# Kernel optimization log

Hardware: AMD Instinct MI355X
Metric: run time of the kernel (lower is better)

## Reference

```python
import jax, jax.numpy as jnp
import numpy as np

B, T, E, A = 16, 512, 256, 8

def setup_inputs() -> dict:
    key = jax.random.key(0)
    k1, k2, k3, k4, k5 = jax.random.split(key, 5)
    sent_feat = jax.random.normal(k1, (B, T, E), dtype=jnp.float32)
    mask = jax.random.randint(k2, (B, T), 0, 2, dtype=jnp.int32)
    atr_scores = jax.random.uniform(k3, (B, A), dtype=jnp.float32)
    W = jax.random.normal(k4, (E, A * E), dtype=jnp.float32) * 0.02  # nn.Linear weight (out, in)
    b = jax.random.normal(k5, (E,), dtype=jnp.float32) * 0.02
    return {"sent_feat": sent_feat, "mask": mask, "atr_scores": atr_scores, "W": W, "b": b}

def reference(sent_feat, mask, atr_scores, W, b):
    Bb, Tt, Ee = sent_feat.shape
    Aa = atr_scores.shape[1]
    sqrt_dim = jnp.float32(np.sqrt(Ee))
    # scale per-attribute copies of the sentence features: (B,A,T,E)
    sf = sent_feat[:, None, :, :] * atr_scores[:, :, None, None]
    sf = sf.reshape(Bb * Aa, Tt, Ee)
    # scaled dot-product scores (B*A, T, T)
    score = jnp.einsum('bte,bse->bts', sf, sf) / sqrt_dim
    # outer-product mask: bmm(mask[:,:,1], mask[:,1,:]) -> bool, repeat over A
    mf = mask.astype(jnp.float32)
    m2 = (mf[:, :, None] * mf[:, None, :]) != 0.0  # (B,T,T)
    m2 = jnp.broadcast_to(m2[:, None, :, :], (Bb, Aa, Tt, Tt)).reshape(Bb * Aa, Tt, Tt)
    # masked_fill_ fills score with 0.0 where mask == 0 (NOT -inf, faithful to source)
    score = jnp.where(m2, score, jnp.float32(0.0))
    # softmax(score - global_max) over last axis
    attn = jax.nn.softmax(score - jnp.max(score), axis=-1)
    attn_out = jnp.einsum('bts,bse->bte', attn, sf)  # (B*A, T, E)
    attn_out = attn_out.reshape(Bb, Tt, Aa * Ee)
    output = attn_out @ W.T + b  # (B, T, E)
    return (output, attn)
```

## Files before the change

### kernel.cpp

```cpp
#include <hip/hip_runtime.h>
#include <hip/hip_bf16.h>


#define Bt 16
#define Tt 512
#define Et 256
#define At 8

typedef __attribute__((ext_vector_type(8))) short short8;
typedef __attribute__((ext_vector_type(4))) float floatx4;

static __device__ __forceinline__ unsigned short f2bf(float x) {
    union { float f; unsigned u; } v; v.f = x;
    unsigned r = v.u + 0x7fffu + ((v.u >> 16) & 1u);
    return (unsigned short)(r >> 16);
}

static __device__ __forceinline__ floatx4 mfma16(short8 a, short8 b, floatx4 c) {
    return __builtin_amdgcn_mfma_f32_16x16x32_bf16(a, b, c, 0, 0, 0);
}

__global__ __launch_bounds__(256) void k_prep_sent(const float* __restrict__ sent,
                                                   unsigned short* __restrict__ sentG,
                                                   unsigned short* __restrict__ sentFB) {
    int bb = blockIdx.z;
    int s0 = blockIdx.x * 32;
    int e0 = blockIdx.y * 32;
    __shared__ float tile[32][33];
    int c  = threadIdx.x & 31;
    int r4 = threadIdx.x >> 5;
    for (int i = 0; i < 4; ++i) {
        int r = r4 + 8 * i;
        tile[r][c] = sent[(bb * Tt + s0 + r) * Et + e0 + c];
    }
    __syncthreads();
    int wv = threadIdx.x >> 6, lane = threadIdx.x & 63, quad = lane >> 4, l16 = lane & 15;
    union { short8 s; unsigned short e[8]; } u;
    if (wv < 2) {
#pragma unroll
        for (int j = 0; j < 8; ++j) u.e[j] = f2bf(tile[wv * 16 + l16][quad * 8 + j]);
        *(short8*)(sentG + (((size_t)(bb * 32 + (s0 >> 4) + wv)) * 8 + (e0 >> 5)) * 512
                   + lane * 8) = u.s;
    } else {
        int h = wv - 2;
#pragma unroll
        for (int j = 0; j < 8; ++j) u.e[j] = f2bf(tile[quad * 8 + j][h * 16 + l16]);
        *(short8*)(sentFB + (((size_t)(bb * 16 + (e0 >> 4) + h)) * 16 + (s0 >> 5)) * 512
                   + lane * 8) = u.s;
    }
}

__global__ __launch_bounds__(256) void k_prep_w(const float* __restrict__ W,
                                                unsigned short* __restrict__ Wp) {
    int nt = blockIdx.x;
    int wave = threadIdx.x >> 6, lane = threadIdx.x & 63, quad = lane >> 4, l16 = lane & 15;
    const int KK = At * Et;
    for (int p = 0; p < 16; ++p) {
        int kc = wave + 4 * p;
        const float* src = W + (size_t)(nt * 16 + l16) * KK + kc * 32 + quad * 8;
        union { short8 s; unsigned short e[8]; } u;
#pragma unroll
        for (int j = 0; j < 8; ++j) u.e[j] = f2bf(src[j]);
        *(short8*)(Wp + (((size_t)nt * 64 + kc) << 9) + lane * 8) = u.s;
    }
}

__global__ __launch_bounds__(256) void k_attnpv(const unsigned short* __restrict__ sentG,
                                                const unsigned short* __restrict__ sentFB,
                                                const int* __restrict__ mask,
                                                const float* __restrict__ atr,
                                                float* __restrict__ attnf,
                                                unsigned short* __restrict__ Xws) {
    int bb = blockIdx.y;
    int t0 = blockIdx.x * 16;
    __shared__ float S[16][516];
    __shared__ float msk[512];
    __shared__ float mrowv[16];
    unsigned short* Pb = (unsigned short*)&S[0][0];
    unsigned short* Xb = Pb + 8192;

    int tid = threadIdx.x;
    for (int i = tid; i < 512; i += 256) msk[i] = (mask[bb * Tt + i] != 0) ? 1.0f : 0.0f;
    if (tid < 16) mrowv[tid] = (mask[bb * Tt + t0 + tid] != 0) ? 1.0f : 0.0f;
    __syncthreads();

    int wv = tid >> 6, lane = tid & 63, quad = lane >> 4, l16 = lane & 15;

    const unsigned short* Gbase = sentG + ((size_t)(bb * 32 + (t0 >> 4)) * 8) * 512 + lane * 8;
    short8 af[8];
#pragma unroll
    for (int kk = 0; kk < 8; ++kk) af[kk] = *(const short8*)(Gbase + kk * 512);

#pragma unroll
    for (int i = 0; i < 8; ++i) {
        int nt = wv * 8 + i;
        const unsigned short* Bb = sentG + ((size_t)(bb * 32 + nt) * 8) * 512 + lane * 8;
        floatx4 c = {0.f, 0.f, 0.f, 0.f};
#pragma unroll
        for (int kk = 0; kk < 8; ++kk)
            c = mfma16(af[kk], *(const short8*)(Bb + kk * 512), c);
#pragma unroll
        for (int r = 0; r < 4; ++r) {
            int cidx = nt * 16 + l16;
            S[quad * 4 + r][cidx] = c[r] * msk[cidx] * mrowv[quad * 4 + r];
        }
    }
    __syncthreads();

    int row = tid >> 4, cl = tid & 15;
    float w[32];
    float wmax = -1e30f;
#pragma unroll
    for (int i4 = 0; i4 < 8; ++i4) {
        float4 v = *(const float4*)&S[row][i4 * 64 + cl * 4];
        w[i4 * 4 + 0] = v.x; w[i4 * 4 + 1] = v.y; w[i4 * 4 + 2] = v.z; w[i4 * 4 + 3] = v.w;
        wmax = fmaxf(wmax, fmaxf(fmaxf(v.x, v.y), fmaxf(v.z, v.w)));
    }
#pragma unroll
    for (int off = 8; off >= 1; off >>= 1) wmax = fmaxf(wmax, __shfl_xor(wmax, off, 64));
    __syncthreads();

    for (int a = 0; a < At; ++a) {
        float av = atr[bb * At + a];
        float coef = av * av * (1.0f / 16.0f);
        float mx = coef * wmax;
        float p[32];
        float sum = 0.f;
#pragma unroll
        for (int j = 0; j < 32; ++j) {
            float e = __expf(fmaf(coef, w[j], -mx));
            p[j] = e;
            sum += e;
        }
#pragma unroll
        for (int off = 8; off >= 1; off >>= 1) sum += __shfl_xor(sum, off, 64);
        float inv = 1.0f / sum;
#pragma unroll
        for (int j = 0; j < 32; ++j) p[j] *= inv;

        float* orow = attnf + ((size_t)(bb * At + a) * Tt + (t0 + row)) * Tt;
#pragma unroll
        for (int i4 = 0; i4 < 8; ++i4) {
            float4 v;
            v.x = p[i4 * 4 + 0]; v.y = p[i4 * 4 + 1];
            v.z = p[i4 * 4 + 2]; v.w = p[i4 * 4 + 3];
            *(float4*)(orow + i4 * 64 + cl * 4) = v;
        }

#pragma unroll
        for (int i4 = 0; i4 < 8; ++i4) {
            unsigned a0 = __float_as_uint(p[i4 * 4 + 0]) + 0x8000u;
            unsigned a1 = __float_as_uint(p[i4 * 4 + 1]) + 0x8000u;
            unsigned a2 = __float_as_uint(p[i4 * 4 + 2]) + 0x8000u;
            unsigned a3 = __float_as_uint(p[i4 * 4 + 3]) + 0x8000u;
            uint2 pk;
            pk.x = __builtin_amdgcn_perm(a1, a0, 0x07060302u);
            pk.y = __builtin_amdgcn_perm(a3, a2, 0x07060302u);
            int h = i4 * 8 + (cl >> 1);
            *(uint2*)(Pb + row * 512 + ((h ^ (row & 7)) << 3) + (cl & 1) * 4) = pk;
        }
        __syncthreads();

        floatx4 pacc[4];
#pragma unroll
        for (int i = 0; i < 4; ++i) pacc[i] = (floatx4){0.f, 0.f, 0.f, 0.f};
        for (int kc = 0; kc < 16; ++kc) {
            short8 afr = *(const short8*)(Pb + l16 * 512 +
                (((kc * 4 + quad) ^ (l16 & 7)) << 3));
#pragma unroll
            for (int i = 0; i < 4; ++i) {
                short8 bfr = *(const short8*)(sentFB +
                    (((size_t)(bb * 16 + wv * 4 + i) * 16 + kc) << 9) + lane * 8);
                pacc[i] = mfma16(afr, bfr, pacc[i]);
            }
        }

#pragma unroll
        for (int i = 0; i < 4; ++i) {
            int e = (wv * 4 + i) * 16 + l16;
#pragma unroll
            for (int r = 0; r < 4; ++r) {
                int tl = quad * 4 + r;
                Xb[(tl >> 3) * 2048 + (tl & 7) * 256 + e] = f2bf(av * pacc[i][r]);
            }
        }
        __syncthreads();

        {
            size_t xbase = ((size_t)bb * Tt + a * 64 + (t0 >> 3)) * 2048;
            int g = tid >> 7, off = (tid & 127) * 16;
            short8 v0 = *(const short8*)(Xb + g * 2048 + off);
            short8 v1 = *(const short8*)(Xb + g * 2048 + off + 8);
            *(short8*)(Xws + xbase + g * 2048 + off) = v0;
            *(short8*)(Xws + xbase + g * 2048 + off + 8) = v1;
        }
    }
}

__global__ __launch_bounds__(256) void k_out(const unsigned short* __restrict__ Xws,
                                             const unsigned short* __restrict__ Wp,
                                             const float* __restrict__ bias,
                                             float* __restrict__ out) {
    int bb = blockIdx.y;
    int tp0 = blockIdx.x * 16;
    int tid = threadIdx.x;
    int wv = tid >> 6, lane = tid & 63, quad = lane >> 4, l16 = lane & 15;

    __shared__ unsigned short Xb[16 * 2048];

    int rhat = tid >> 4;
    int hb   = tid & 15;
    const unsigned short* src = Xws + ((size_t)bb * Tt + tp0 + rhat) * 2048;
#pragma unroll
    for (int p = 0; p < 16; ++p) {
        int h = hb + 16 * p;
        short8 v = *(const short8*)(src + h * 8);
        *(short8*)(Xb + rhat * 2048 + ((h ^ (rhat & 7)) << 3)) = v;
    }
    __syncthreads();

    floatx4 oacc[4];
#pragma unroll
    for (int i = 0; i < 4; ++i) oacc[i] = (floatx4){0.f, 0.f, 0.f, 0.f};

    const int KK = At * Et;
    for (int k0 = 0; k0 < KK; k0 += 32) {
        short8 afr = *(const short8*)(Xb + l16 * 2048 +
            ((((k0 >> 3) + quad) ^ (l16 & 7)) << 3));
#pragma unroll
        for (int i = 0; i < 4; ++i) {
            short8 bf = *(const short8*)(Wp +
                (((size_t)(wv * 4 + i) * 64 + (k0 >> 5)) << 9) + lane * 8);
            oacc[i] = mfma16(afr, bf, oacc[i]);
        }
    }
#pragma unroll
    for (int i = 0; i < 4; ++i) {
        int n = (wv * 4 + i) * 16 + l16;
        float bv = bias[n];
#pragma unroll
        for (int r = 0; r < 4; ++r) {
            int tp = tp0 + quad * 4 + r;
            out[((size_t)bb * Tt + tp) * Et + n] = oacc[i][r] + bv;
        }
    }
}

extern "C" void kernel_launch(void* const* d_in, const int* in_sizes, int n_in,
                              void* d_out, int out_size, void* d_ws, size_t ws_size,
                              hipStream_t stream) {
    const float* sent = (const float*)d_in[0];
    const int*   mask = (const int*)d_in[1];
    const float* atr  = (const float*)d_in[2];
    const float* W    = (const float*)d_in[3];
    const float* bias = (const float*)d_in[4];

    float* out0  = (float*)d_out;
    float* attnf = out0 + (size_t)Bt * Tt * Et;

    char* ws = (char*)d_ws;
    unsigned short* sentG  = (unsigned short*)(ws);
    unsigned short* sentFB = (unsigned short*)(ws + 4194304);
    unsigned short* Wp     = (unsigned short*)(ws + 8388608);
    unsigned short* Xws    = (unsigned short*)(ws + 9437184);

    hipLaunchKernelGGL(k_prep_sent, dim3(Tt / 32, Et / 32, Bt), dim3(256), 0, stream,
                       sent, sentG, sentFB);
    hipLaunchKernelGGL(k_prep_w, dim3(16), dim3(256), 0, stream, W, Wp);
    hipLaunchKernelGGL(k_attnpv, dim3(Tt / 16, Bt), dim3(256), 0, stream,
                       sentG, sentFB, mask, atr, attnf, Xws);
    hipLaunchKernelGGL(k_out, dim3(Tt / 16, Bt), dim3(256), 0, stream,
                       Xws, Wp, bias, out0);
}
```

Measured before the change: 220.6 us.

## Split attention over attribute halves and widen output GEMM blocks to 512 threads

The attention kernel grid gains a z dimension of 2, so each block handles 4 of the 8 attributes. This doubles block count (1024 instead of 512) for better CU occupancy, at the cost of recomputing the QK^T scores and row max in both halves. The output projection kernel moves to 512 threads with 2 N-tiles per wave instead of 4, which spreads the work across more waves. __syncthreads calls are replaced with a custom barrier that waits only on LDS counters, which lets global stores stay in flight across the barrier.

```diff
diff --git a/kernel.cpp b/kernel.cpp
--- a/kernel.cpp
+++ b/kernel.cpp
@@ -18,6 +18,13 @@
 
 static __device__ __forceinline__ floatx4 mfma16(short8 a, short8 b, floatx4 c) {
     return __builtin_amdgcn_mfma_f32_16x16x32_bf16(a, b, c, 0, 0, 0);
+}
+
+static __device__ __forceinline__ void barrier_lds() {
+    __builtin_amdgcn_sched_barrier(0);
+    asm volatile("s_waitcnt lgkmcnt(0)" ::: "memory");
+    __builtin_amdgcn_s_barrier();
+    __builtin_amdgcn_sched_barrier(0);
 }
 
 __global__ __launch_bounds__(256) void k_prep_sent(const float* __restrict__ sent,
@@ -73,6 +80,7 @@
                                                 unsigned short* __restrict__ Xws) {
     int bb = blockIdx.y;
     int t0 = blockIdx.x * 16;
+    int a0 = blockIdx.z * 4;
     __shared__ float S[16][516];
     __shared__ float msk[512];
     __shared__ float mrowv[16];
@@ -82,7 +90,7 @@
     int tid = threadIdx.x;
     for (int i = tid; i < 512; i += 256) msk[i] = (mask[bb * Tt + i] != 0) ? 1.0f : 0.0f;
     if (tid < 16) mrowv[tid] = (mask[bb * Tt + t0 + tid] != 0) ? 1.0f : 0.0f;
-    __syncthreads();
+    barrier_lds();
 
     int wv = tid >> 6, lane = tid & 63, quad = lane >> 4, l16 = lane & 15;
 
@@ -105,7 +113,7 @@
             S[quad * 4 + r][cidx] = c[r] * msk[cidx] * mrowv[quad * 4 + r];
         }
     }
-    __syncthreads();
+    barrier_lds();
 
     int row = tid >> 4, cl = tid & 15;
     float w[32];
@@ -118,9 +126,9 @@
     }
 #pragma unroll
     for (int off = 8; off >= 1; off >>= 1) wmax = fmaxf(wmax, __shfl_xor(wmax, off, 64));
-    __syncthreads();
-
-    for (int a = 0; a < At; ++a) {
+    barrier_lds();
+
+    for (int a = a0; a < a0 + 4; ++a) {
         float av = atr[bb * At + a];
         float coef = av * av * (1.0f / 16.0f);
         float mx = coef * wmax;
@@ -149,17 +157,17 @@
 
 #pragma unroll
         for (int i4 = 0; i4 < 8; ++i4) {
-            unsigned a0 = __float_as_uint(p[i4 * 4 + 0]) + 0x8000u;
-            unsigned a1 = __float_as_uint(p[i4 * 4 + 1]) + 0x8000u;
-            unsigned a2 = __float_as_uint(p[i4 * 4 + 2]) + 0x8000u;
-            unsigned a3 = __float_as_uint(p[i4 * 4 + 3]) + 0x8000u;
+            unsigned b0 = __float_as_uint(p[i4 * 4 + 0]) + 0x8000u;
+            unsigned b1 = __float_as_uint(p[i4 * 4 + 1]) + 0x8000u;
+            unsigned b2 = __float_as_uint(p[i4 * 4 + 2]) + 0x8000u;
+            unsigned b3 = __float_as_uint(p[i4 * 4 + 3]) + 0x8000u;
             uint2 pk;
-            pk.x = __builtin_amdgcn_perm(a1, a0, 0x07060302u);
-            pk.y = __builtin_amdgcn_perm(a3, a2, 0x07060302u);
+            pk.x = __builtin_amdgcn_perm(b1, b0, 0x07060302u);
+            pk.y = __builtin_amdgcn_perm(b3, b2, 0x07060302u);
             int h = i4 * 8 + (cl >> 1);
             *(uint2*)(Pb + row * 512 + ((h ^ (row & 7)) << 3) + (cl & 1) * 4) = pk;
         }
-        __syncthreads();
+        barrier_lds();
 
         floatx4 pacc[4];
 #pragma unroll
@@ -184,7 +192,7 @@
                 Xb[(tl >> 3) * 2048 + (tl & 7) * 256 + e] = f2bf(av * pacc[i][r]);
             }
         }
-        __syncthreads();
+        barrier_lds();
 
         {
             size_t xbase = ((size_t)bb * Tt + a * 64 + (t0 >> 3)) * 2048;
@@ -197,7 +205,7 @@
     }
 }
 
-__global__ __launch_bounds__(256) void k_out(const unsigned short* __restrict__ Xws,
+__global__ __launch_bounds__(512) void k_out(const unsigned short* __restrict__ Xws,
                                              const unsigned short* __restrict__ Wp,
                                              const float* __restrict__ bias,
                                              float* __restrict__ out) {
@@ -208,35 +216,35 @@
 
     __shared__ unsigned short Xb[16 * 2048];
 
-    int rhat = tid >> 4;
-    int hb   = tid & 15;
+    int rhat = tid >> 5;
+    int hb   = tid & 31;
     const unsigned short* src = Xws + ((size_t)bb * Tt + tp0 + rhat) * 2048;
 #pragma unroll
-    for (int p = 0; p < 16; ++p) {
-        int h = hb + 16 * p;
+    for (int p = 0; p < 8; ++p) {
+        int h = hb + 32 * p;
         short8 v = *(const short8*)(src + h * 8);
         *(short8*)(Xb + rhat * 2048 + ((h ^ (rhat & 7)) << 3)) = v;
     }
     __syncthreads();
 
-    floatx4 oacc[4];
-#pragma unroll
-    for (int i = 0; i < 4; ++i) oacc[i] = (floatx4){0.f, 0.f, 0.f, 0.f};
+    floatx4 oacc[2];
+#pragma unroll
+    for (int i = 0; i < 2; ++i) oacc[i] = (floatx4){0.f, 0.f, 0.f, 0.f};
 
     const int KK = At * Et;
     for (int k0 = 0; k0 < KK; k0 += 32) {
         short8 afr = *(const short8*)(Xb + l16 * 2048 +
             ((((k0 >> 3) + quad) ^ (l16 & 7)) << 3));
 #pragma unroll
-        for (int i = 0; i < 4; ++i) {
+        for (int i = 0; i < 2; ++i) {
             short8 bf = *(const short8*)(Wp +
-                (((size_t)(wv * 4 + i) * 64 + (k0 >> 5)) << 9) + lane * 8);
+                (((size_t)(wv * 2 + i) * 64 + (k0 >> 5)) << 9) + lane * 8);
             oacc[i] = mfma16(afr, bf, oacc[i]);
         }
     }
 #pragma unroll
-    for (int i = 0; i < 4; ++i) {
-        int n = (wv * 4 + i) * 16 + l16;
+    for (int i = 0; i < 2; ++i) {
+        int n = (wv * 2 + i) * 16 + l16;
         float bv = bias[n];
 #pragma unroll
         for (int r = 0; r < 4; ++r) {
@@ -267,8 +275,8 @@
     hipLaunchKernelGGL(k_prep_sent, dim3(Tt / 32, Et / 32, Bt), dim3(256), 0, stream,
                        sent, sentG, sentFB);
     hipLaunchKernelGGL(k_prep_w, dim3(16), dim3(256), 0, stream, W, Wp);
-    hipLaunchKernelGGL(k_attnpv, dim3(Tt / 16, Bt), dim3(256), 0, stream,
+    hipLaunchKernelGGL(k_attnpv, dim3(Tt / 16, Bt, 2), dim3(256), 0, stream,
                        sentG, sentFB, mask, atr, attnf, Xws);
-    hipLaunchKernelGGL(k_out, dim3(Tt / 16, Bt), dim3(256), 0, stream,
+    hipLaunchKernelGGL(k_out, dim3(Tt / 16, Bt), dim3(512), 0, stream,
                        Xws, Wp, bias, out0);
 }
```

New measurement: 251.6 us. +14.1%, slower.
